# Optimization experiments

Measured on AMD Instinct MI355X. Metric: run time of the kernel, lower is better.

## Reference

```python
import jax, jax.numpy as jnp
import numpy as np

# FreqEncoder constants (from init_kwargs)
X_DIM = 3
MIN_DEG = 0.0
MAX_DEG = 8.0
NUM_SCALES = 8            # max_deg - min_deg
RES = 128                 # 2 ** log2_res
NUM_CH = 8                # num_feats (channels per grid)
STD = 0.001
P = 262144                # number of sample points


def setup_inputs() -> dict:
    key = jax.random.key(0)
    k1, k2 = jax.random.split(key)
    x = jax.random.uniform(k1, (P, X_DIM), dtype=jnp.float32)
    # learned 1D grids: [num_scales*2*x_dim, num_channels, res]
    features = jax.random.normal(k2, (NUM_SCALES * 2 * X_DIM, NUM_CH, RES), dtype=jnp.float32) * STD
    return {"x": x, "features": features}


def reference(x, features):
    S, D, C, res = NUM_SCALES, X_DIM, NUM_CH, RES
    N = S * 2 * D  # number of 1D grids
    p = x.shape[0]

    # scales = 2 ** linspace(min_deg, max_deg, num_scales)  (matches torch.linspace)
    scales = 2.0 ** jnp.linspace(MIN_DEG, MAX_DEG, S).astype(x.dtype)  # [S]

    xb = x[:, None, :] * scales[None, :, None]                     # [P, S, D]
    latent = jnp.sin(jnp.stack([xb, xb + 0.5 * jnp.pi], axis=-2))  # [P, S, 2, D]

    # values in [-1, 1] used as grid_sample y-coords; one grid per (s, phase, d)
    v = latent.reshape(p, N).T                                     # [N, P]

    # align_corners=True bilinear unnormalization along the res axis
    pos = (v + 1.0) * 0.5 * (res - 1)                              # [N, P] in [0, res-1]
    i0f = jnp.floor(pos)
    frac = pos - i0f                                               # [N, P]
    i0 = jnp.clip(i0f, 0, res - 1).astype(jnp.int32)
    i1 = jnp.clip(i0 + 1, 0, res - 1)

    idx0 = jnp.broadcast_to(i0[:, None, :], (N, C, p))
    idx1 = jnp.broadcast_to(i1[:, None, :], (N, C, p))
    f0 = jnp.take_along_axis(features, idx0, axis=2)               # [N, C, P]
    f1 = jnp.take_along_axis(features, idx1, axis=2)               # [N, C, P]
    fs = f0 * (1.0 - frac[:, None, :]) + f1 * frac[:, None, :]     # [N, C, P]

    # [N, C, P] -> [S, 2, D, C, P] -> [P, C, S, 2, D], add residual, flatten
    fs = fs.reshape(S, 2, D, C, p).transpose(4, 3, 0, 1, 2)
    out = (fs + latent[:, None, :, :, :]).reshape(p, C * S * 2 * D)

    # use_identity=True: prepend raw coordinates
    return jnp.concatenate([x, out], axis=-1)                      # [P, 3 + 384]
```

## Files before the change

kernel.cpp:

```cpp
#include <hip/hip_runtime.h>
#include <hip/hip_bf16.h>
#include <stdint.h>


constexpr int P_PTS = 262144;
constexpr int S_SC  = 8;
constexpr int D_DIM = 3;
constexpr int C_CH  = 8;
constexpr int RES   = 128;
constexpr int N_GR  = S_SC * 2 * D_DIM;
constexpr int OW    = 3 + C_CH * N_GR;
constexpr int KPB   = 32;
constexpr int CHUNKS = 8;
constexpr int PPB   = KPB * CHUNKS;
constexpr int BLK   = 1024;

constexpr float ENC_SCALE = 256.0f;
constexpr float DEC_SCALE = 1.0f / 256.0f;
constexpr float INV_2PI   = 0.15915494309189535f;

constexpr int LDS_TABLE_B = N_GR * RES * 16;
constexpr int LDS_SOUT_B  = KPB * OW * 4;
constexpr int LDS_SX_B    = PPB * D_DIM * 4;
constexpr int LDS_TOTAL_B = LDS_TABLE_B + LDS_SOUT_B + LDS_SX_B;

typedef float f32x2 __attribute__((ext_vector_type(2)));

__device__ uint4 g_pair[N_GR * RES];

__global__ __launch_bounds__(256) void feat_pack_kernel(const float* __restrict__ f) {
    int t = blockIdx.x * 256 + threadIdx.x;
    if (t >= N_GR * RES) return;
    int n = t / RES, i = t % RES;
    int ia = i;
    int ib = min(i + 1, RES - 1);

    uint32_t d[4];
    {
        float a = f[(n * C_CH + 0) * RES + ia] * ENC_SCALE;
        float b = f[(n * C_CH + 1) * RES + ia] * ENC_SCALE;
        float c = f[(n * C_CH + 2) * RES + ia] * ENC_SCALE;
        float e = f[(n * C_CH + 3) * RES + ia] * ENC_SCALE;
        int lo = __builtin_amdgcn_cvt_pk_fp8_f32(a, b, 0, false);
        d[0] = (uint32_t)__builtin_amdgcn_cvt_pk_fp8_f32(c, e, lo, true);
    }
    {
        float a = f[(n * C_CH + 4) * RES + ia] * ENC_SCALE;
        float b = f[(n * C_CH + 5) * RES + ia] * ENC_SCALE;
        float c = f[(n * C_CH + 6) * RES + ia] * ENC_SCALE;
        float e = f[(n * C_CH + 7) * RES + ia] * ENC_SCALE;
        int lo = __builtin_amdgcn_cvt_pk_fp8_f32(a, b, 0, false);
        d[1] = (uint32_t)__builtin_amdgcn_cvt_pk_fp8_f32(c, e, lo, true);
    }
    {
        float a = f[(n * C_CH + 0) * RES + ib] * ENC_SCALE;
        float b = f[(n * C_CH + 1) * RES + ib] * ENC_SCALE;
        float c = f[(n * C_CH + 2) * RES + ib] * ENC_SCALE;
        float e = f[(n * C_CH + 3) * RES + ib] * ENC_SCALE;
        int lo = __builtin_amdgcn_cvt_pk_fp8_f32(a, b, 0, false);
        d[2] = (uint32_t)__builtin_amdgcn_cvt_pk_fp8_f32(c, e, lo, true);
    }
    {
        float a = f[(n * C_CH + 4) * RES + ib] * ENC_SCALE;
        float b = f[(n * C_CH + 5) * RES + ib] * ENC_SCALE;
        float c = f[(n * C_CH + 6) * RES + ib] * ENC_SCALE;
        float e = f[(n * C_CH + 7) * RES + ib] * ENC_SCALE;
        int lo = __builtin_amdgcn_cvt_pk_fp8_f32(a, b, 0, false);
        d[3] = (uint32_t)__builtin_amdgcn_cvt_pk_fp8_f32(c, e, lo, true);
    }
    g_pair[t] = make_uint4(d[0], d[1], d[2], d[3]);
}

__global__ __launch_bounds__(1024) void freq_encode_kernel(const float* __restrict__ x,
                                                           float* __restrict__ out) {
    extern __shared__ char smem[];
    uint4* ld_pair = reinterpret_cast<uint4*>(smem);
    float* s_out   = reinterpret_cast<float*>(smem + LDS_TABLE_B);
    float* s_x     = reinterpret_cast<float*>(smem + LDS_TABLE_B + LDS_SOUT_B);

    const int tid   = threadIdx.x;
    const int pbase = blockIdx.x * PPB;

    for (int i = tid; i < N_GR * RES; i += BLK) ld_pair[i] = g_pair[i];
    for (int i = tid; i < PPB * D_DIM; i += BLK) s_x[i] = x[(size_t)pbase * D_DIM + i];
    __syncthreads();

    for (int ch = 0; ch < CHUNKS; ++ch) {
        const int p0l = ch * KPB;

        if (tid < KPB * D_DIM) {
            s_out[(tid / D_DIM) * OW + (tid % D_DIM)] = s_x[p0l * D_DIM + tid];
        }

        for (int u = tid; u < KPB * N_GR; u += BLK) {
            int pl = u / N_GR;
            int n  = u % N_GR;
            int s  = n / (2 * D_DIM);
            int r  = n % (2 * D_DIM);
            int ph = r / D_DIM;
            int d  = r % D_DIM;

            float xv    = s_x[(p0l + pl) * D_DIM + d];
            float scale = exp2f((float)s * (8.0f / 7.0f));
            float rv    = fmaf(xv * scale, INV_2PI, ph ? 0.25f : 0.0f);
            float lat   = __builtin_amdgcn_sinf(__builtin_amdgcn_fractf(rv));

            float pos  = (lat + 1.0f) * 63.5f;
            float i0f  = floorf(pos);
            float frac = pos - i0f;
            int   i0   = (int)i0f;
            i0 = max(0, min(i0, RES - 1));

            uint4 pk = ld_pair[n * RES + i0];

            f32x2 a01 = __builtin_amdgcn_cvt_pk_f32_fp8(pk.x, false);
            f32x2 a23 = __builtin_amdgcn_cvt_pk_f32_fp8(pk.x, true);
            f32x2 a45 = __builtin_amdgcn_cvt_pk_f32_fp8(pk.y, false);
            f32x2 a67 = __builtin_amdgcn_cvt_pk_f32_fp8(pk.y, true);
            f32x2 b01 = __builtin_amdgcn_cvt_pk_f32_fp8(pk.z, false);
            f32x2 b23 = __builtin_amdgcn_cvt_pk_f32_fp8(pk.z, true);
            f32x2 b45 = __builtin_amdgcn_cvt_pk_f32_fp8(pk.w, false);
            f32x2 b67 = __builtin_amdgcn_cvt_pk_f32_fp8(pk.w, true);

            float omd = (1.0f - frac) * DEC_SCALE;
            float frd = frac * DEC_SCALE;

            float* dst = &s_out[pl * OW + 3 + n];
            dst[0 * N_GR] = fmaf(a01[0], omd, fmaf(b01[0], frd, lat));
            dst[1 * N_GR] = fmaf(a01[1], omd, fmaf(b01[1], frd, lat));
            dst[2 * N_GR] = fmaf(a23[0], omd, fmaf(b23[0], frd, lat));
            dst[3 * N_GR] = fmaf(a23[1], omd, fmaf(b23[1], frd, lat));
            dst[4 * N_GR] = fmaf(a45[0], omd, fmaf(b45[0], frd, lat));
            dst[5 * N_GR] = fmaf(a45[1], omd, fmaf(b45[1], frd, lat));
            dst[6 * N_GR] = fmaf(a67[0], omd, fmaf(b67[0], frd, lat));
            dst[7 * N_GR] = fmaf(a67[1], omd, fmaf(b67[1], frd, lat));
        }
        __syncthreads();

        constexpr int NV = KPB * OW / 4;
        const float4* src = reinterpret_cast<const float4*>(s_out);
        float4*       dst = reinterpret_cast<float4*>(out + ((size_t)pbase + p0l) * OW);
        for (int i = tid; i < NV; i += BLK) {
            dst[i] = src[i];
        }
        __syncthreads();
    }
}

extern "C" void kernel_launch(void* const* d_in, const int* in_sizes, int n_in,
                              void* d_out, int out_size, void* d_ws, size_t ws_size,
                              hipStream_t stream) {
    const float* x    = (const float*)d_in[0];
    const float* feat = (const float*)d_in[1];
    float*       out  = (float*)d_out;

    int n_pairs = N_GR * RES;
    feat_pack_kernel<<<(n_pairs + 255) / 256, 256, 0, stream>>>(feat);

    freq_encode_kernel<<<P_PTS / PPB, BLK, LDS_TOTAL_B, stream>>>(x, out);
}
```

Before: 88.80 us.

## Double-buffer output staging and shrink LDS feature table to single taps

Splits the LDS output staging area into two buffers so the global store of one chunk overlaps the compute of the next, halving the number of block barriers per chunk. The feature table now holds single fp8 taps (8 bytes) instead of precomputed pairs (16 bytes), so each lookup issues two 8-byte LDS reads instead of one 16-byte read. This frees LDS to pay for the second staging buffer, at the cost of extra LDS read instructions and possible bank conflicts.

New measurement: 88.80 us. Within noise of the previous version (-0.0%).

```diff
diff --git a/kernel.cpp b/kernel.cpp
--- a/kernel.cpp
+++ b/kernel.cpp
@@ -19,79 +19,59 @@
 constexpr float DEC_SCALE = 1.0f / 256.0f;
 constexpr float INV_2PI   = 0.15915494309189535f;
 
-constexpr int LDS_TABLE_B = N_GR * RES * 16;
+constexpr int LDS_TABLE_B = N_GR * RES * 8;
 constexpr int LDS_SOUT_B  = KPB * OW * 4;
 constexpr int LDS_SX_B    = PPB * D_DIM * 4;
-constexpr int LDS_TOTAL_B = LDS_TABLE_B + LDS_SOUT_B + LDS_SX_B;
+constexpr int LDS_TOTAL_B = LDS_TABLE_B + 2 * LDS_SOUT_B + LDS_SX_B;
 
 typedef float f32x2 __attribute__((ext_vector_type(2)));
 
-__device__ uint4 g_pair[N_GR * RES];
+__device__ uint2 g_tap[N_GR * RES];
 
 __global__ __launch_bounds__(256) void feat_pack_kernel(const float* __restrict__ f) {
     int t = blockIdx.x * 256 + threadIdx.x;
     if (t >= N_GR * RES) return;
     int n = t / RES, i = t % RES;
-    int ia = i;
-    int ib = min(i + 1, RES - 1);
 
-    uint32_t d[4];
+    uint32_t d0, d1;
     {
-        float a = f[(n * C_CH + 0) * RES + ia] * ENC_SCALE;
-        float b = f[(n * C_CH + 1) * RES + ia] * ENC_SCALE;
-        float c = f[(n * C_CH + 2) * RES + ia] * ENC_SCALE;
-        float e = f[(n * C_CH + 3) * RES + ia] * ENC_SCALE;
+        float a = f[(n * C_CH + 0) * RES + i] * ENC_SCALE;
+        float b = f[(n * C_CH + 1) * RES + i] * ENC_SCALE;
+        float c = f[(n * C_CH + 2) * RES + i] * ENC_SCALE;
+        float e = f[(n * C_CH + 3) * RES + i] * ENC_SCALE;
         int lo = __builtin_amdgcn_cvt_pk_fp8_f32(a, b, 0, false);
-        d[0] = (uint32_t)__builtin_amdgcn_cvt_pk_fp8_f32(c, e, lo, true);
+        d0 = (uint32_t)__builtin_amdgcn_cvt_pk_fp8_f32(c, e, lo, true);
     }
     {
-        float a = f[(n * C_CH + 4) * RES + ia] * ENC_SCALE;
-        float b = f[(n * C_CH + 5) * RES + ia] * ENC_SCALE;
-        float c = f[(n * C_CH + 6) * RES + ia] * ENC_SCALE;
-        float e = f[(n * C_CH + 7) * RES + ia] * ENC_SCALE;
+        float a = f[(n * C_CH + 4) * RES + i] * ENC_SCALE;
+        float b = f[(n * C_CH + 5) * RES + i] * ENC_SCALE;
+        float c = f[(n * C_CH + 6) * RES + i] * ENC_SCALE;
+        float e = f[(n * C_CH + 7) * RES + i] * ENC_SCALE;
         int lo = __builtin_amdgcn_cvt_pk_fp8_f32(a, b, 0, false);
-        d[1] = (uint32_t)__builtin_amdgcn_cvt_pk_fp8_f32(c, e, lo, true);
+        d1 = (uint32_t)__builtin_amdgcn_cvt_pk_fp8_f32(c, e, lo, true);
     }
-    {
-        float a = f[(n * C_CH + 0) * RES + ib] * ENC_SCALE;
-        float b = f[(n * C_CH + 1) * RES + ib] * ENC_SCALE;
-        float c = f[(n * C_CH + 2) * RES + ib] * ENC_SCALE;
-        float e = f[(n * C_CH + 3) * RES + ib] * ENC_SCALE;
-        int lo = __builtin_amdgcn_cvt_pk_fp8_f32(a, b, 0, false);
-        d[2] = (uint32_t)__builtin_amdgcn_cvt_pk_fp8_f32(c, e, lo, true);
-    }
-    {
-        float a = f[(n * C_CH + 4) * RES + ib] * ENC_SCALE;
-        float b = f[(n * C_CH + 5) * RES + ib] * ENC_SCALE;
-        float c = f[(n * C_CH + 6) * RES + ib] * ENC_SCALE;
-        float e = f[(n * C_CH + 7) * RES + ib] * ENC_SCALE;
-        int lo = __builtin_amdgcn_cvt_pk_fp8_f32(a, b, 0, false);
-        d[3] = (uint32_t)__builtin_amdgcn_cvt_pk_fp8_f32(c, e, lo, true);
-    }
-    g_pair[t] = make_uint4(d[0], d[1], d[2], d[3]);
+    g_tap[t] = make_uint2(d0, d1);
 }
 
 __global__ __launch_bounds__(1024) void freq_encode_kernel(const float* __restrict__ x,
                                                            float* __restrict__ out) {
     extern __shared__ char smem[];
-    uint4* ld_pair = reinterpret_cast<uint4*>(smem);
-    float* s_out   = reinterpret_cast<float*>(smem + LDS_TABLE_B);
-    float* s_x     = reinterpret_cast<float*>(smem + LDS_TABLE_B + LDS_SOUT_B);
+    uint2* ld_tap = reinterpret_cast<uint2*>(smem);
+    float* s_out0 = reinterpret_cast<float*>(smem + LDS_TABLE_B);
+    float* s_out1 = reinterpret_cast<float*>(smem + LDS_TABLE_B + LDS_SOUT_B);
+    float* s_x    = reinterpret_cast<float*>(smem + LDS_TABLE_B + 2 * LDS_SOUT_B);
 
     const int tid   = threadIdx.x;
     const int pbase = blockIdx.x * PPB;
 
-    for (int i = tid; i < N_GR * RES; i += BLK) ld_pair[i] = g_pair[i];
+    for (int i = tid; i < N_GR * RES; i += BLK) ld_tap[i] = g_tap[i];
     for (int i = tid; i < PPB * D_DIM; i += BLK) s_x[i] = x[(size_t)pbase * D_DIM + i];
     __syncthreads();
 
-    for (int ch = 0; ch < CHUNKS; ++ch) {
-        const int p0l = ch * KPB;
-
+    auto do_compute = [&](int p0l, float* sbuf) {
         if (tid < KPB * D_DIM) {
-            s_out[(tid / D_DIM) * OW + (tid % D_DIM)] = s_x[p0l * D_DIM + tid];
+            sbuf[(tid / D_DIM) * OW + (tid % D_DIM)] = s_x[p0l * D_DIM + tid];
         }
-
         for (int u = tid; u < KPB * N_GR; u += BLK) {
             int pl = u / N_GR;
             int n  = u % N_GR;
@@ -110,22 +90,24 @@
             float frac = pos - i0f;
             int   i0   = (int)i0f;
             i0 = max(0, min(i0, RES - 1));
+            int   i1   = min(i0 + 1, RES - 1);
 
-            uint4 pk = ld_pair[n * RES + i0];
+            uint2 t0 = ld_tap[n * RES + i0];
+            uint2 t1 = ld_tap[n * RES + i1];
 
-            f32x2 a01 = __builtin_amdgcn_cvt_pk_f32_fp8(pk.x, false);
-            f32x2 a23 = __builtin_amdgcn_cvt_pk_f32_fp8(pk.x, true);
-            f32x2 a45 = __builtin_amdgcn_cvt_pk_f32_fp8(pk.y, false);
-            f32x2 a67 = __builtin_amdgcn_cvt_pk_f32_fp8(pk.y, true);
-            f32x2 b01 = __builtin_amdgcn_cvt_pk_f32_fp8(pk.z, false);
-            f32x2 b23 = __builtin_amdgcn_cvt_pk_f32_fp8(pk.z, true);
-            f32x2 b45 = __builtin_amdgcn_cvt_pk_f32_fp8(pk.w, false);
-            f32x2 b67 = __builtin_amdgcn_cvt_pk_f32_fp8(pk.w, true);
+            f32x2 a01 = __builtin_amdgcn_cvt_pk_f32_fp8(t0.x, false);
+            f32x2 a23 = __builtin_amdgcn_cvt_pk_f32_fp8(t0.x, true);
+            f32x2 a45 = __builtin_amdgcn_cvt_pk_f32_fp8(t0.y, false);
+            f32x2 a67 = __builtin_amdgcn_cvt_pk_f32_fp8(t0.y, true);
+            f32x2 b01 = __builtin_amdgcn_cvt_pk_f32_fp8(t1.x, false);
+            f32x2 b23 = __builtin_amdgcn_cvt_pk_f32_fp8(t1.x, true);
+            f32x2 b45 = __builtin_amdgcn_cvt_pk_f32_fp8(t1.y, false);
+            f32x2 b67 = __builtin_amdgcn_cvt_pk_f32_fp8(t1.y, true);
 
             float omd = (1.0f - frac) * DEC_SCALE;
             float frd = frac * DEC_SCALE;
 
-            float* dst = &s_out[pl * OW + 3 + n];
+            float* dst = &sbuf[pl * OW + 3 + n];
             dst[0 * N_GR] = fmaf(a01[0], omd, fmaf(b01[0], frd, lat));
             dst[1 * N_GR] = fmaf(a01[1], omd, fmaf(b01[1], frd, lat));
             dst[2 * N_GR] = fmaf(a23[0], omd, fmaf(b23[0], frd, lat));
@@ -135,16 +117,27 @@
             dst[6 * N_GR] = fmaf(a67[0], omd, fmaf(b67[0], frd, lat));
             dst[7 * N_GR] = fmaf(a67[1], omd, fmaf(b67[1], frd, lat));
         }
-        __syncthreads();
+    };
 
+    auto do_store = [&](int p0l, const float* sbuf) {
         constexpr int NV = KPB * OW / 4;
-        const float4* src = reinterpret_cast<const float4*>(s_out);
+        const float4* src = reinterpret_cast<const float4*>(sbuf);
         float4*       dst = reinterpret_cast<float4*>(out + ((size_t)pbase + p0l) * OW);
         for (int i = tid; i < NV; i += BLK) {
             dst[i] = src[i];
         }
+    };
+
+    do_compute(0, s_out0);
+    __syncthreads();
+    for (int ch = 1; ch < CHUNKS; ++ch) {
+        float* cur  = (ch & 1) ? s_out1 : s_out0;
+        float* prev = (ch & 1) ? s_out0 : s_out1;
+        do_store((ch - 1) * KPB, prev);
+        do_compute(ch * KPB, cur);
         __syncthreads();
     }
+    do_store((CHUNKS - 1) * KPB, ((CHUNKS - 1) & 1) ? s_out1 : s_out0);
 }
 
 extern "C" void kernel_launch(void* const* d_in, const int* in_sizes, int n_in,
@@ -154,8 +147,8 @@
     const float* feat = (const float*)d_in[1];
     float*       out  = (float*)d_out;
 
-    int n_pairs = N_GR * RES;
-    feat_pack_kernel<<<(n_pairs + 255) / 256, 256, 0, stream>>>(feat);
+    int n_taps = N_GR * RES;
+    feat_pack_kernel<<<(n_taps + 255) / 256, 256, 0, stream>>>(feat);
 
     freq_encode_kernel<<<P_PTS / PPB, BLK, LDS_TOTAL_B, stream>>>(x, out);
 }
```
